# Kernel optimization log

Measured on AMD Instinct MI355X. Metric: run time of the kernel, lower is better.

Reference implementation:

```python
import jax, jax.numpy as jnp
import numpy as np

I_DIM, H_DIM, SEQ, OUT = 2048, 2048, 4096, 2048

def setup_inputs() -> dict:
    key = jax.random.key(0)
    ks = jax.random.split(key, 8)
    s_i = 1.0 / np.sqrt(H_DIM)
    return {
        "input_seq": jax.random.normal(ks[0], (1, SEQ, I_DIM), dtype=jnp.float32),
        "W_ih": jax.random.uniform(ks[1], (4 * H_DIM, I_DIM), minval=-s_i, maxval=s_i, dtype=jnp.float32),
        "W_hh": jax.random.uniform(ks[2], (4 * H_DIM, H_DIM), minval=-s_i, maxval=s_i, dtype=jnp.float32),
        "b_ih": jax.random.uniform(ks[3], (4 * H_DIM,), minval=-s_i, maxval=s_i, dtype=jnp.float32),
        "b_hh": jax.random.uniform(ks[4], (4 * H_DIM,), minval=-s_i, maxval=s_i, dtype=jnp.float32),
        "W_fc": jax.random.uniform(ks[5], (OUT, H_DIM), minval=-s_i, maxval=s_i, dtype=jnp.float32),
        "b_fc": jax.random.uniform(ks[6], (OUT,), minval=-s_i, maxval=s_i, dtype=jnp.float32),
    }

def _lstm_last_h(x, W_ih, W_hh, b_ih, b_hh):
    # x: [B, S, I]. PyTorch gate order: i, f, g, o along the 4H axis.
    B, S, _ = x.shape
    H = W_hh.shape[1]
    # Precompute input contribution for all timesteps: [B, S, 4H]
    xg = jnp.einsum('bsi,gi->bsg', x, W_ih) + b_ih + b_hh

    def step(carry, xg_t):
        h, c = carry  # [B, H] each
        g = xg_t + h @ W_hh.T  # [B, 4H]
        i_g = jax.nn.sigmoid(g[:, 0 * H:1 * H])
        f_g = jax.nn.sigmoid(g[:, 1 * H:2 * H])
        g_g = jnp.tanh(g[:, 2 * H:3 * H])
        o_g = jax.nn.sigmoid(g[:, 3 * H:4 * H])
        c = f_g * c + i_g * g_g
        h = o_g * jnp.tanh(c)
        return (h, c), None

    h0 = jnp.zeros((B, H), dtype=x.dtype)
    c0 = jnp.zeros((B, H), dtype=x.dtype)
    (h_last, _), _ = jax.lax.scan(step, (h0, c0), jnp.swapaxes(xg, 0, 1))
    return h_last  # [B, H]

def reference(input_seq, W_ih, W_hh, b_ih, b_hh, W_fc, b_fc):
    h_last = _lstm_last_h(input_seq, W_ih, W_hh, b_ih, b_hh)
    # Original does predictions.view(1, -1) then fc; valid only for batch=1.
    pred = h_last.reshape(1, -1) @ W_fc.T + b_fc  # [1, OUT]
    return pred
```

## Files before the change

kernel.cpp:

```cpp
#include <hip/hip_runtime.h>
#include <hip/hip_bf16.h>
#include <hip/hip_fp16.h>

#define SEQ   4096
#define IDIM  2048
#define HDIM  2048
#define G4    8192
#define NBLK  256
#define NREP  8

typedef __attribute__((ext_vector_type(8))) short short8;
typedef __attribute__((ext_vector_type(4))) float f32x4;

__device__ __forceinline__ float fast_sig(float x) {
    float e = __builtin_amdgcn_exp2f(-1.4426950408889634f * x);
    return __builtin_amdgcn_rcpf(1.0f + e);
}
__device__ __forceinline__ float fast_tanh(float x) {
    float e = __builtin_amdgcn_exp2f(2.8853900817779268f * x);
    return 1.0f - 2.0f * __builtin_amdgcn_rcpf(e + 1.0f);
}
__device__ __forceinline__ unsigned short f2h(float f) {
    __half h = __float2half_rn(f);
    union { __half h; unsigned short s; } c; c.h = h; return c.s;
}
__device__ __forceinline__ float h2f(unsigned short u) {
    union { unsigned short s; __half h; } c; c.s = u; return __half2float(c.h);
}

#define GM 128
#define GN 128
#define GK 32
#define APAD 40

__global__ __launch_bounds__(256, 2)
void xg_gemm(const float* __restrict__ x, const float* __restrict__ Wih,
             const float* __restrict__ bih, const float* __restrict__ bhh,
             __hip_bfloat16* __restrict__ xg)
{
    __shared__ __hip_bfloat16 As[GM][APAD];
    __shared__ __hip_bfloat16 Bs[GN][APAD];

    const int t  = threadIdx.x;
    const int g0 = blockIdx.x * GN;
    const int s0 = blockIdx.y * GM;
    const int w  = t >> 6, L = t & 63;
    const int quad = L >> 4, lane16 = L & 15;
    const int wm = w >> 1, wn = w & 1;

    f32x4 acc[4][4];
#pragma unroll
    for (int mt = 0; mt < 4; ++mt)
#pragma unroll
        for (int nt = 0; nt < 4; ++nt) acc[mt][nt] = (f32x4){0.f, 0.f, 0.f, 0.f};

    const int srow = t >> 1, shalf = t & 1;
    const float* xp = x   + (size_t)(s0 + srow) * IDIM + 16 * shalf;
    const float* wp = Wih + (size_t)(g0 + srow) * IDIM + 16 * shalf;

    for (int k0 = 0; k0 < IDIM; k0 += GK) {
        float4 a0 = *(const float4*)(xp + k0);
        float4 a1 = *(const float4*)(xp + k0 + 4);
        float4 a2 = *(const float4*)(xp + k0 + 8);
        float4 a3 = *(const float4*)(xp + k0 + 12);
        float4 b0 = *(const float4*)(wp + k0);
        float4 b1 = *(const float4*)(wp + k0 + 4);
        float4 b2 = *(const float4*)(wp + k0 + 8);
        float4 b3 = *(const float4*)(wp + k0 + 12);
        __syncthreads();
        {
            union { __hip_bfloat16 h[8]; uint4 u; } pk;
            pk.h[0]=__float2bfloat16(a0.x); pk.h[1]=__float2bfloat16(a0.y);
            pk.h[2]=__float2bfloat16(a0.z); pk.h[3]=__float2bfloat16(a0.w);
            pk.h[4]=__float2bfloat16(a1.x); pk.h[5]=__float2bfloat16(a1.y);
            pk.h[6]=__float2bfloat16(a1.z); pk.h[7]=__float2bfloat16(a1.w);
            *(uint4*)&As[srow][16 * shalf] = pk.u;
            pk.h[0]=__float2bfloat16(a2.x); pk.h[1]=__float2bfloat16(a2.y);
            pk.h[2]=__float2bfloat16(a2.z); pk.h[3]=__float2bfloat16(a2.w);
            pk.h[4]=__float2bfloat16(a3.x); pk.h[5]=__float2bfloat16(a3.y);
            pk.h[6]=__float2bfloat16(a3.z); pk.h[7]=__float2bfloat16(a3.w);
            *(uint4*)&As[srow][16 * shalf + 8] = pk.u;
            pk.h[0]=__float2bfloat16(b0.x); pk.h[1]=__float2bfloat16(b0.y);
            pk.h[2]=__float2bfloat16(b0.z); pk.h[3]=__float2bfloat16(b0.w);
            pk.h[4]=__float2bfloat16(b1.x); pk.h[5]=__float2bfloat16(b1.y);
            pk.h[6]=__float2bfloat16(b1.z); pk.h[7]=__float2bfloat16(b1.w);
            *(uint4*)&Bs[srow][16 * shalf] = pk.u;
            pk.h[0]=__float2bfloat16(b2.x); pk.h[1]=__float2bfloat16(b2.y);
            pk.h[2]=__float2bfloat16(b2.z); pk.h[3]=__float2bfloat16(b2.w);
            pk.h[4]=__float2bfloat16(b3.x); pk.h[5]=__float2bfloat16(b3.y);
            pk.h[6]=__float2bfloat16(b3.z); pk.h[7]=__float2bfloat16(b3.w);
            *(uint4*)&Bs[srow][16 * shalf + 8] = pk.u;
        }
        __syncthreads();

        short8 af[4], bf[4];
#pragma unroll
        for (int mt = 0; mt < 4; ++mt)
            af[mt] = *(const short8*)&As[wm * 64 + mt * 16 + lane16][quad * 8];
#pragma unroll
        for (int nt = 0; nt < 4; ++nt)
            bf[nt] = *(const short8*)&Bs[wn * 64 + nt * 16 + lane16][quad * 8];
#pragma unroll
        for (int mt = 0; mt < 4; ++mt)
#pragma unroll
            for (int nt = 0; nt < 4; ++nt)
                acc[mt][nt] = __builtin_amdgcn_mfma_f32_16x16x32_bf16(
                                  af[mt], bf[nt], acc[mt][nt], 0, 0, 0);
    }

#pragma unroll
    for (int nt = 0; nt < 4; ++nt) {
        const int g = g0 + wn * 64 + nt * 16 + lane16;
        const float bias = bih[g] + bhh[g];
#pragma unroll
        for (int mt = 0; mt < 4; ++mt) {
#pragma unroll
            for (int r = 0; r < 4; ++r) {
                const int so = s0 + wm * 64 + mt * 16 + quad * 4 + r;
                xg[(size_t)so * G4 + g] = __float2bfloat16(acc[mt][nt][r] + bias);
            }
        }
    }
}

__global__ __launch_bounds__(256, 1)
void lstm_rec(const float* __restrict__ Whh,
              const __hip_bfloat16* __restrict__ xg,
              float* __restrict__ hout,
              unsigned long long* __restrict__ msg)
{
    __shared__ float hsh[2][HDIM];
    __shared__ int   flag[4];

    const int t  = threadIdx.x;
    const int b  = blockIdx.x;
    const int w  = t >> 6;
    const int L  = t & 63;
    const int hi = L & 1;
    const int go = (L >> 1) & 3;
    const int rb = b & (NREP - 1);

    float4 wv[8][8];
#pragma unroll
    for (int r = 0; r < 8; ++r) {
        const float* rp = Whh + (size_t)((r >> 1) * HDIM + 8 * b + 2 * w + (r & 1)) * HDIM + 4 * L;
#pragma unroll
        for (int jj = 0; jj < 8; ++jj) wv[r][jj] = *(const float4*)(rp + 256 * jj);
    }

    if (t < 4) flag[t] = -1;
    float creg = 0.0f;
    float xq0, xq1, xq2, xq3;
    {
        const size_t xb = (size_t)(8 * b + 2 * w + hi);
        xq0 = __bfloat162float(xg[xb]);
        xq1 = __bfloat162float(xg[xb + HDIM]);
        xq2 = __bfloat162float(xg[xb + 2 * HDIM]);
        xq3 = __bfloat162float(xg[xb + 3 * HDIM]);
    }
    __syncthreads();

    for (int s = 0; s < SEQ; ++s) {
        const int pb = s & 1;

        float f0,f1,f2,f3,f4,f5,f6,f7;
        if (s == 0) {
            f0=f1=f2=f3=f4=f5=f6=f7 = 0.0f;
        } else {
            const unsigned long long* p0 = &msg[(size_t)((pb * NREP + rb) * 4 + 0) * NBLK + t];
            const unsigned long long* p1 = &msg[(size_t)((pb * NREP + rb) * 4 + 1) * NBLK + t];
            const unsigned long long* p2 = &msg[(size_t)((pb * NREP + rb) * 4 + 2) * NBLK + t];
            const unsigned long long* p3 = &msg[(size_t)((pb * NREP + rb) * 4 + 3) * NBLK + t];
            const unsigned tgt = (unsigned)s;
            unsigned long long v0, v1, v2, v3;
            do {
                v0 = __hip_atomic_load(p0, __ATOMIC_RELAXED, __HIP_MEMORY_SCOPE_AGENT);
                v1 = __hip_atomic_load(p1, __ATOMIC_RELAXED, __HIP_MEMORY_SCOPE_AGENT);
                v2 = __hip_atomic_load(p2, __ATOMIC_RELAXED, __HIP_MEMORY_SCOPE_AGENT);
                v3 = __hip_atomic_load(p3, __ATOMIC_RELAXED, __HIP_MEMORY_SCOPE_AGENT);
            } while ((unsigned)(v0 & 0xFFFFu) < tgt ||
                     (unsigned)(v1 & 0xFFFFu) < tgt ||
                     (unsigned)(v2 & 0xFFFFu) < tgt ||
                     (unsigned)(v3 & 0xFFFFu) < tgt);
            f0 = h2f((unsigned short)(v0 >> 16));
            f1 = h2f((unsigned short)(v0 >> 32));
            f2 = h2f((unsigned short)(v1 >> 16));
            f3 = h2f((unsigned short)(v1 >> 32));
            f4 = h2f((unsigned short)(v2 >> 16));
            f5 = h2f((unsigned short)(v2 >> 32));
            f6 = h2f((unsigned short)(v3 >> 16));
            f7 = h2f((unsigned short)(v3 >> 32));
        }
        float4 hv0 = { f0, f1, f2, f3 };
        float4 hv1 = { f4, f5, f6, f7 };
        *(float4*)&hsh[pb][8 * t]     = hv0;
        *(float4*)&hsh[pb][8 * t + 4] = hv1;
        if (L == 0)
            __hip_atomic_store(&flag[w], s, __ATOMIC_RELEASE, __HIP_MEMORY_SCOPE_WORKGROUP);

        float a0=0.f,a1=0.f,a2=0.f,a3=0.f,a4=0.f,a5=0.f,a6=0.f,a7=0.f;
#pragma unroll
        for (int c = 0; c < 4; ++c) {
            if (c != w) {
                while (__hip_atomic_load(&flag[c], __ATOMIC_ACQUIRE,
                                         __HIP_MEMORY_SCOPE_WORKGROUP) < s) {}
            }
#pragma unroll
            for (int u = 0; u < 2; ++u) {
                const int jj = 2 * c + u;
                float4 hv = *(const float4*)&hsh[pb][4 * (L + 64 * jj)];
                a0 += wv[0][jj].x*hv.x; a0 += wv[0][jj].y*hv.y; a0 += wv[0][jj].z*hv.z; a0 += wv[0][jj].w*hv.w;
                a1 += wv[1][jj].x*hv.x; a1 += wv[1][jj].y*hv.y; a1 += wv[1][jj].z*hv.z; a1 += wv[1][jj].w*hv.w;
                a2 += wv[2][jj].x*hv.x; a2 += wv[2][jj].y*hv.y; a2 += wv[2][jj].z*hv.z; a2 += wv[2][jj].w*hv.w;
                a3 += wv[3][jj].x*hv.x; a3 += wv[3][jj].y*hv.y; a3 += wv[3][jj].z*hv.z; a3 += wv[3][jj].w*hv.w;
                a4 += wv[4][jj].x*hv.x; a4 += wv[4][jj].y*hv.y; a4 += wv[4][jj].z*hv.z; a4 += wv[4][jj].w*hv.w;
                a5 += wv[5][jj].x*hv.x; a5 += wv[5][jj].y*hv.y; a5 += wv[5][jj].z*hv.z; a5 += wv[5][jj].w*hv.w;
                a6 += wv[6][jj].x*hv.x; a6 += wv[6][jj].y*hv.y; a6 += wv[6][jj].z*hv.z; a6 += wv[6][jj].w*hv.w;
                a7 += wv[7][jj].x*hv.x; a7 += wv[7][jj].y*hv.y; a7 += wv[7][jj].z*hv.z; a7 += wv[7][jj].w*hv.w;
            }
        }

        float b0v = (hi ? a1 : a0) + __shfl_xor(hi ? a0 : a1, 1, 64);
        float b1v = (hi ? a3 : a2) + __shfl_xor(hi ? a2 : a3, 1, 64);
        float b2v = (hi ? a5 : a4) + __shfl_xor(hi ? a4 : a5, 1, 64);
        float b3v = (hi ? a7 : a6) + __shfl_xor(hi ? a6 : a7, 1, 64);
        const int bit1 = (L >> 1) & 1;
        float c0v = (bit1 ? b1v : b0v) + __shfl_xor(bit1 ? b0v : b1v, 2, 64);
        float c1v = (bit1 ? b3v : b2v) + __shfl_xor(bit1 ? b2v : b3v, 2, 64);
        const int bit2 = (L >> 2) & 1;
        float dv  = (bit2 ? c1v : c0v) + __shfl_xor(bit2 ? c0v : c1v, 4, 64);
        dv += __shfl_xor(dv, 8, 64);
        dv += __shfl_xor(dv, 16, 64);
        dv += __shfl_xor(dv, 32, 64);

        float q0 = dv;
        float q1 = __shfl_xor(dv, 2, 64);
        float q2 = __shfl_xor(dv, 4, 64);
        float q3 = __shfl_xor(dv, 6, 64);
        float t0 = (go & 1) ? q1 : q0, t1 = (go & 1) ? q0 : q1;
        float t2 = (go & 1) ? q3 : q2, t3 = (go & 1) ? q2 : q3;
        float pi = ((go & 2) ? t2 : t0) + xq0;
        float pf = ((go & 2) ? t3 : t1) + xq1;
        float pg = ((go & 2) ? t0 : t2) + xq2;
        float po = ((go & 2) ? t1 : t3) + xq3;

        float cn = fast_sig(pf) * creg + fast_sig(pi) * fast_tanh(pg);
        creg = cn;
        float h = fast_sig(po) * fast_tanh(cn);
        if (s == SEQ - 1 && L < 2) hout[8 * b + 2 * w + L] = h;

        if (s + 1 < SEQ) {
            const int p = (s + 1) & 1;
            float h0 = __shfl(h, 0, 64);
            float h1 = __shfl(h, 1, 64);
            if (L < NREP) {
                unsigned long long u = (unsigned long long)(unsigned short)(s + 1)
                    | ((unsigned long long)f2h(h0) << 16)
                    | ((unsigned long long)f2h(h1) << 32);
                (void)__hip_atomic_exchange(
                        &msg[(size_t)((p * NREP + L) * 4 + w) * NBLK + b], u,
                        __ATOMIC_RELAXED, __HIP_MEMORY_SCOPE_AGENT);
            }
            const size_t xb = (size_t)(s + 1) * G4 + 8 * b + 2 * w + hi;
            xq0 = __bfloat162float(xg[xb]);
            xq1 = __bfloat162float(xg[xb + HDIM]);
            xq2 = __bfloat162float(xg[xb + 2 * HDIM]);
            xq3 = __bfloat162float(xg[xb + 3 * HDIM]);
        }
    }
}

__global__ __launch_bounds__(64)
void fc_kernel(const float* __restrict__ h, const float* __restrict__ Wfc,
               const float* __restrict__ bfc, float* __restrict__ out)
{
    const int o = blockIdx.x;
    const int L = threadIdx.x;
    const float* wr = Wfc + (size_t)o * HDIM;
    float s = 0.0f;
#pragma unroll
    for (int jj = 0; jj < 8; ++jj) {
        float4 wvv = *(const float4*)(wr + 4 * (L + 64 * jj));
        float4 hv  = *(const float4*)(h  + 4 * (L + 64 * jj));
        s += wvv.x * hv.x + wvv.y * hv.y + wvv.z * hv.z + wvv.w * hv.w;
    }
#pragma unroll
    for (int mask = 1; mask <= 32; mask <<= 1) s += __shfl_xor(s, mask, 64);
    if (L == 0) out[o] = s + bfc[o];
}

extern "C" void kernel_launch(void* const* d_in, const int* in_sizes, int n_in,
                              void* d_out, int out_size, void* d_ws, size_t ws_size,
                              hipStream_t stream)
{
    (void)in_sizes; (void)n_in; (void)out_size; (void)ws_size;
    const float* x   = (const float*)d_in[0];
    const float* Wih = (const float*)d_in[1];
    const float* Whh = (const float*)d_in[2];
    const float* bih = (const float*)d_in[3];
    const float* bhh = (const float*)d_in[4];
    const float* Wfc = (const float*)d_in[5];
    const float* bfc = (const float*)d_in[6];
    float* out = (float*)d_out;

    __hip_bfloat16* xg       = (__hip_bfloat16*)d_ws;
    float* hout              = (float*)((char*)d_ws + (size_t)SEQ * G4 * sizeof(__hip_bfloat16));
    unsigned long long* msg  = (unsigned long long*)(hout + HDIM);

    (void)hipMemsetAsync(msg, 0, (size_t)2 * NREP * 4 * NBLK * sizeof(unsigned long long), stream);

    dim3 g1(G4 / GN, SEQ / GM);
    hipLaunchKernelGGL(xg_gemm, g1, dim3(256), 0, stream, x, Wih, bih, bhh, xg);

    float* hout_arg = hout;
    unsigned long long* msg_arg = msg;
    void* args[] = { (void*)&Whh, (void*)&xg, (void*)&hout_arg, (void*)&msg_arg };
    hipError_t ce = hipLaunchCooperativeKernel((const void*)lstm_rec, dim3(NBLK), dim3(256),
                                               args, 0, stream);
    if (ce != hipSuccess) {
        hipLaunchKernelGGL(lstm_rec, dim3(NBLK), dim3(256), 0, stream, Whh, xg, hout, msg);
    }

    hipLaunchKernelGGL(fc_kernel, dim3(2048), dim3(64), 0, stream, hout, Wfc, bfc, out);
}
```

Before: 11.69 ms.

## Start each wave on its own h chunk and simplify gate reduction shuffles

Permutes the order in which each wave walks the four shared-memory h chunks, starting with its own (w^i) so it can compute before waiting on other waves' flags, and reorders the register-held weights to match. Replaces the transposing butterfly reduction plus the gate-redistribution shuffles with four full xor reductions, which removes a dependent shuffle stage and the select logic but issues more shuffles overall. It also uses a min-based spin condition and a single xor shuffle to gather the h pair. The aim is to shorten the per-timestep critical path of the recurrent loop.

```diff
diff --git a/kernel.cpp b/kernel.cpp
--- a/kernel.cpp
+++ b/kernel.cpp
@@ -137,7 +137,6 @@
     const int w  = t >> 6;
     const int L  = t & 63;
     const int hi = L & 1;
-    const int go = (L >> 1) & 3;
     const int rb = b & (NREP - 1);
 
     float4 wv[8][8];
@@ -145,7 +144,12 @@
     for (int r = 0; r < 8; ++r) {
         const float* rp = Whh + (size_t)((r >> 1) * HDIM + 8 * b + 2 * w + (r & 1)) * HDIM + 4 * L;
 #pragma unroll
-        for (int jj = 0; jj < 8; ++jj) wv[r][jj] = *(const float4*)(rp + 256 * jj);
+        for (int i = 0; i < 4; ++i) {
+            const int c = w ^ i;
+#pragma unroll
+            for (int u = 0; u < 2; ++u)
+                wv[r][2 * i + u] = *(const float4*)(rp + 512 * c + 256 * u);
+        }
     }
 
     if (t < 4) flag[t] = -1;
@@ -178,10 +182,8 @@
                 v1 = __hip_atomic_load(p1, __ATOMIC_RELAXED, __HIP_MEMORY_SCOPE_AGENT);
                 v2 = __hip_atomic_load(p2, __ATOMIC_RELAXED, __HIP_MEMORY_SCOPE_AGENT);
                 v3 = __hip_atomic_load(p3, __ATOMIC_RELAXED, __HIP_MEMORY_SCOPE_AGENT);
-            } while ((unsigned)(v0 & 0xFFFFu) < tgt ||
-                     (unsigned)(v1 & 0xFFFFu) < tgt ||
-                     (unsigned)(v2 & 0xFFFFu) < tgt ||
-                     (unsigned)(v3 & 0xFFFFu) < tgt);
+            } while (min(min((unsigned)(v0 & 0xFFFFu), (unsigned)(v1 & 0xFFFFu)),
+                         min((unsigned)(v2 & 0xFFFFu), (unsigned)(v3 & 0xFFFFu))) < tgt);
             f0 = h2f((unsigned short)(v0 >> 16));
             f1 = h2f((unsigned short)(v0 >> 32));
             f2 = h2f((unsigned short)(v1 >> 16));
@@ -200,49 +202,42 @@
 
         float a0=0.f,a1=0.f,a2=0.f,a3=0.f,a4=0.f,a5=0.f,a6=0.f,a7=0.f;
 #pragma unroll
-        for (int c = 0; c < 4; ++c) {
-            if (c != w) {
+        for (int i = 0; i < 4; ++i) {
+            const int c = w ^ i;
+            if (i != 0) {
                 while (__hip_atomic_load(&flag[c], __ATOMIC_ACQUIRE,
                                          __HIP_MEMORY_SCOPE_WORKGROUP) < s) {}
             }
 #pragma unroll
             for (int u = 0; u < 2; ++u) {
-                const int jj = 2 * c + u;
-                float4 hv = *(const float4*)&hsh[pb][4 * (L + 64 * jj)];
-                a0 += wv[0][jj].x*hv.x; a0 += wv[0][jj].y*hv.y; a0 += wv[0][jj].z*hv.z; a0 += wv[0][jj].w*hv.w;
-                a1 += wv[1][jj].x*hv.x; a1 += wv[1][jj].y*hv.y; a1 += wv[1][jj].z*hv.z; a1 += wv[1][jj].w*hv.w;
-                a2 += wv[2][jj].x*hv.x; a2 += wv[2][jj].y*hv.y; a2 += wv[2][jj].z*hv.z; a2 += wv[2][jj].w*hv.w;
-                a3 += wv[3][jj].x*hv.x; a3 += wv[3][jj].y*hv.y; a3 += wv[3][jj].z*hv.z; a3 += wv[3][jj].w*hv.w;
-                a4 += wv[4][jj].x*hv.x; a4 += wv[4][jj].y*hv.y; a4 += wv[4][jj].z*hv.z; a4 += wv[4][jj].w*hv.w;
-                a5 += wv[5][jj].x*hv.x; a5 += wv[5][jj].y*hv.y; a5 += wv[5][jj].z*hv.z; a5 += wv[5][jj].w*hv.w;
-                a6 += wv[6][jj].x*hv.x; a6 += wv[6][jj].y*hv.y; a6 += wv[6][jj].z*hv.z; a6 += wv[6][jj].w*hv.w;
-                a7 += wv[7][jj].x*hv.x; a7 += wv[7][jj].y*hv.y; a7 += wv[7][jj].z*hv.z; a7 += wv[7][jj].w*hv.w;
+                const int q = 2 * i + u;
+                float4 hv = *(const float4*)&hsh[pb][4 * L + 512 * c + 256 * u];
+                a0 += wv[0][q].x*hv.x; a0 += wv[0][q].y*hv.y; a0 += wv[0][q].z*hv.z; a0 += wv[0][q].w*hv.w;
+                a1 += wv[1][q].x*hv.x; a1 += wv[1][q].y*hv.y; a1 += wv[1][q].z*hv.z; a1 += wv[1][q].w*hv.w;
+                a2 += wv[2][q].x*hv.x; a2 += wv[2][q].y*hv.y; a2 += wv[2][q].z*hv.z; a2 += wv[2][q].w*hv.w;
+                a3 += wv[3][q].x*hv.x; a3 += wv[3][q].y*hv.y; a3 += wv[3][q].z*hv.z; a3 += wv[3][q].w*hv.w;
+                a4 += wv[4][q].x*hv.x; a4 += wv[4][q].y*hv.y; a4 += wv[4][q].z*hv.z; a4 += wv[4][q].w*hv.w;
+                a5 += wv[5][q].x*hv.x; a5 += wv[5][q].y*hv.y; a5 += wv[5][q].z*hv.z; a5 += wv[5][q].w*hv.w;
+                a6 += wv[6][q].x*hv.x; a6 += wv[6][q].y*hv.y; a6 += wv[6][q].z*hv.z; a6 += wv[6][q].w*hv.w;
+                a7 += wv[7][q].x*hv.x; a7 += wv[7][q].y*hv.y; a7 += wv[7][q].z*hv.z; a7 += wv[7][q].w*hv.w;
             }
         }
 
-        float b0v = (hi ? a1 : a0) + __shfl_xor(hi ? a0 : a1, 1, 64);
-        float b1v = (hi ? a3 : a2) + __shfl_xor(hi ? a2 : a3, 1, 64);
-        float b2v = (hi ? a5 : a4) + __shfl_xor(hi ? a4 : a5, 1, 64);
-        float b3v = (hi ? a7 : a6) + __shfl_xor(hi ? a6 : a7, 1, 64);
-        const int bit1 = (L >> 1) & 1;
-        float c0v = (bit1 ? b1v : b0v) + __shfl_xor(bit1 ? b0v : b1v, 2, 64);
-        float c1v = (bit1 ? b3v : b2v) + __shfl_xor(bit1 ? b2v : b3v, 2, 64);
-        const int bit2 = (L >> 2) & 1;
-        float dv  = (bit2 ? c1v : c0v) + __shfl_xor(bit2 ? c0v : c1v, 4, 64);
-        dv += __shfl_xor(dv, 8, 64);
-        dv += __shfl_xor(dv, 16, 64);
-        dv += __shfl_xor(dv, 32, 64);
-
-        float q0 = dv;
-        float q1 = __shfl_xor(dv, 2, 64);
-        float q2 = __shfl_xor(dv, 4, 64);
-        float q3 = __shfl_xor(dv, 6, 64);
-        float t0 = (go & 1) ? q1 : q0, t1 = (go & 1) ? q0 : q1;
-        float t2 = (go & 1) ? q3 : q2, t3 = (go & 1) ? q2 : q3;
-        float pi = ((go & 2) ? t2 : t0) + xq0;
-        float pf = ((go & 2) ? t3 : t1) + xq1;
-        float pg = ((go & 2) ? t0 : t2) + xq2;
-        float po = ((go & 2) ? t1 : t3) + xq3;
+        float g0v = (hi ? a1 : a0) + __shfl_xor(hi ? a0 : a1, 1, 64);
+        float g1v = (hi ? a3 : a2) + __shfl_xor(hi ? a2 : a3, 1, 64);
+        float g2v = (hi ? a5 : a4) + __shfl_xor(hi ? a4 : a5, 1, 64);
+        float g3v = (hi ? a7 : a6) + __shfl_xor(hi ? a6 : a7, 1, 64);
+#pragma unroll
+        for (int m = 2; m <= 32; m <<= 1) {
+            g0v += __shfl_xor(g0v, m, 64);
+            g1v += __shfl_xor(g1v, m, 64);
+            g2v += __shfl_xor(g2v, m, 64);
+            g3v += __shfl_xor(g3v, m, 64);
+        }
+        float pi = g0v + xq0;
+        float pf = g1v + xq1;
+        float pg = g2v + xq2;
+        float po = g3v + xq3;
 
         float cn = fast_sig(pf) * creg + fast_sig(pi) * fast_tanh(pg);
         creg = cn;
@@ -251,8 +246,9 @@
 
         if (s + 1 < SEQ) {
             const int p = (s + 1) & 1;
-            float h0 = __shfl(h, 0, 64);
-            float h1 = __shfl(h, 1, 64);
+            float hp = __shfl_xor(h, 1, 64);
+            float h0 = hi ? hp : h;
+            float h1 = hi ? h : hp;
             if (L < NREP) {
                 unsigned long long u = (unsigned long long)(unsigned short)(s + 1)
                     | ((unsigned long long)f2h(h0) << 16)
```

Result: slower. 13.05 ms (+11.6%).
